# Kernel tuning notes

Measured on AMD Instinct MI355X. Metric: run time of the kernel, lower is better.

## Reference

```python
import jax, jax.numpy as jnp
import numpy as np

N = 10000
E = 640000


def setup_inputs() -> dict:
    key = jax.random.key(0)
    k = jax.random.split(key, 6)
    x = jax.random.normal(k[0], (N, 128), dtype=jnp.float32)
    edge_index = jax.random.randint(k[1], (2, E), 0, N, dtype=jnp.int64)
    # Linear weights stored as [in, out] (torch stores [out, in]; math is x @ W.T + b)
    w1 = jax.random.normal(k[2], (128, 128), dtype=jnp.float32) * 0.05
    b1 = jax.random.normal(k[3], (128,), dtype=jnp.float32) * 0.05
    w2 = jax.random.normal(k[4], (128, 128), dtype=jnp.float32) * 0.05
    b2 = jax.random.normal(k[5], (128,), dtype=jnp.float32) * 0.05
    return {"x": x, "edge_index": edge_index, "w1": w1, "b1": b1, "w2": w2, "b2": b2}


def gin_conv(x, src, dst, w, b, eps=0.0):
    # aggregate: out[i] = sum over edges (src->dst=i) of x[src]
    agg = jax.ops.segment_sum(x[src], dst, num_segments=N)  # [N, d]
    h = (1.0 + eps) * x + agg
    return h @ w + b


def reference(x, edge_index, w1, b1, w2, b2):
    src, dst = edge_index[0], edge_index[1]
    h = gin_conv(x, src, dst, w1, b1)
    h = jax.nn.relu(h)
    h = gin_conv(h, src, dst, w2, b2)
    return jax.nn.log_softmax(h, axis=1)
```

## Files before the change

kernel.cpp:

```cpp
#include <hip/hip_runtime.h>
#include <cstdint>

#define NNODES 10000
#define FDIM 128
#define MAXDEG 192
#define NPB 40
#define NBIN 256
#define BINCAP 4096
#define SENT16 0x27102710u

typedef _Float16 h2v  __attribute__((ext_vector_type(2)));
typedef _Float16 f16x8 __attribute__((ext_vector_type(8)));
typedef float    f32x4 __attribute__((ext_vector_type(4)));

__device__ __align__(16)  int            g_binoff[NBIN];
__device__ __align__(16)  unsigned       g_binbuf[NBIN * BINCAP];
__device__ __align__(16)  int            g_cnt[NNODES];
__device__ __align__(16)  unsigned short g_bkt[NNODES * MAXDEG];
__device__ __align__(256) unsigned g_xh [(NNODES + 1) * FDIM / 2];
__device__ __align__(256) unsigned g_h1h[(NNODES + 1) * FDIM / 2];
__device__ __align__(16)  unsigned g_wf[2 * 8192];

__device__ inline h2v as_h2(unsigned u) { return __builtin_bit_cast(h2v, u); }
__device__ inline unsigned as_u(h2v v) { return __builtin_bit_cast(unsigned, v); }
__device__ inline unsigned pack_f16x2(float a, float b) {
  h2v v; v[0] = (_Float16)a; v[1] = (_Float16)b;
  return as_u(v);
}
__device__ inline void vadd4(uint4& a, const uint4& b) {
  a.x = as_u(as_h2(a.x) + as_h2(b.x));
  a.y = as_u(as_h2(a.y) + as_h2(b.y));
  a.z = as_u(as_h2(a.z) + as_h2(b.z));
  a.w = as_u(as_h2(a.w) + as_h2(b.w));
}

__global__ __launch_bounds__(512) void prep1_kernel(
    const float* __restrict__ x, const int* __restrict__ ei,
    const float* __restrict__ w1, const float* __restrict__ w2,
    int E_, int PBLK) {
  const int bid = blockIdx.x, tid = threadIdx.x;
  if (bid < PBLK) {
    __shared__ int lcnt[NBIN], lbase[NBIN];
    if (tid < NBIN) lcnt[tid] = 0;
    __syncthreads();
    int dv[8], sv[8], rk[8], bn[8];
#pragma unroll
    for (int k = 0; k < 8; ++k) {
      int e = bid * 4096 + k * 512 + tid;
      dv[k] = (e < E_) ? ei[E_ + e] : -1;
      sv[k] = (e < E_) ? ei[e] : 0;
    }
#pragma unroll
    for (int k = 0; k < 8; ++k) {
      if (dv[k] >= 0) {
        bn[k] = (unsigned)dv[k] / NPB;
        rk[k] = atomicAdd(&lcnt[bn[k]], 1);
      }
    }
    __syncthreads();
    if (tid < NBIN && lcnt[tid] > 0)
      lbase[tid] = atomicAdd(&g_binoff[tid], lcnt[tid]);
    __syncthreads();
#pragma unroll
    for (int k = 0; k < 8; ++k) {
      if (dv[k] >= 0) {
        int pos = lbase[bn[k]] + rk[k];
        if (pos < BINCAP)
          g_binbuf[bn[k] * BINCAP + pos] =
              ((unsigned)(dv[k] - bn[k] * NPB) << 16) | (unsigned)sv[k];
      }
    }
  } else if (bid < PBLK + 625) {
    int i = (bid - PBLK) * 512 + tid;
    if (i < NNODES * 32) {
      float4 v = *(const float4*)(x + 4 * (size_t)i);
      uint2 o; o.x = pack_f16x2(v.x, v.y); o.y = pack_f16x2(v.z, v.w);
      *(uint2*)(g_xh + 2 * (size_t)i) = o;
    }
  } else {
    int idx = (bid - PBLK - 625) * 512 + tid;
    if (idx < 4096) {
      const float* w = (idx >= 2048) ? w2 : w1;
      int s = idx & 2047;
      int sl = s & 63, nk = s >> 6;
      int n = nk >> 2, kc = nk & 3;
      int kbase = kc * 32 + (sl >> 4) * 8;
      int f = n * 16 + (sl & 15);
      unsigned d0 = pack_f16x2(w[(size_t)(kbase + 0) * FDIM + f],
                               w[(size_t)(kbase + 1) * FDIM + f]);
      unsigned d1 = pack_f16x2(w[(size_t)(kbase + 2) * FDIM + f],
                               w[(size_t)(kbase + 3) * FDIM + f]);
      unsigned d2 = pack_f16x2(w[(size_t)(kbase + 4) * FDIM + f],
                               w[(size_t)(kbase + 5) * FDIM + f]);
      unsigned d3 = pack_f16x2(w[(size_t)(kbase + 6) * FDIM + f],
                               w[(size_t)(kbase + 7) * FDIM + f]);
      *(uint4*)(g_wf + (idx >> 11) * 8192 + 4 * s) = make_uint4(d0, d1, d2, d3);
    }
  }
}

__global__ __launch_bounds__(512) void prep2_kernel() {
  __shared__ int lcnt[NPB];
  __shared__ __align__(16) unsigned short lbkt[NPB * MAXDEG];

  const int bid = blockIdx.x, tid = threadIdx.x;
  const int lo = bid * NPB;
  const int nnr = NNODES - lo;
  const int nn = (nnr < 0) ? 0 : ((nnr < NPB) ? nnr : NPB);
  for (int i = tid; i < NPB; i += 512) lcnt[i] = 0;
  {
    const uint4 sent = make_uint4(SENT16, SENT16, SENT16, SENT16);
    uint4* lb4 = (uint4*)lbkt;
    for (int i = tid; i < NPB * MAXDEG / 8; i += 512) lb4[i] = sent;
  }
  __syncthreads();

  int cnt = g_binoff[bid];
  if (cnt > BINCAP) cnt = BINCAP;
  const unsigned* buf = g_binbuf + (size_t)bid * BINCAP;
  for (int i = tid; i < cnt; i += 512) {
    unsigned p = buf[i];
    int rel = (int)(p >> 16);
    if (rel < nn) {
      int q = atomicAdd(&lcnt[rel], 1);
      if (q < MAXDEG) lbkt[rel * MAXDEG + q] = (unsigned short)(p & 0xffffu);
    }
  }
  __syncthreads();

  for (int i = tid; i < nn; i += 512)
    g_cnt[lo + i] = (lcnt[i] > MAXDEG) ? MAXDEG : lcnt[i];
  const int nq = nn * (MAXDEG / 8);
  const uint4* srcq = (const uint4*)lbkt;
  uint4* dstq = (uint4*)(g_bkt + (size_t)lo * MAXDEG);
  for (int i = tid; i < nq; i += 512) dstq[i] = srcq[i];
  if (tid == 0) g_binoff[bid] = 0;
}

template <int MODE>
__global__ __launch_bounds__(512) void gin_layer_kernel(
    const float* __restrict__ bvec,
    float* __restrict__ out_g) {
  const unsigned* __restrict__ xh = (MODE == 0) ? g_xh : g_h1h;

  __shared__ __align__(16) unsigned al[16 * 68];
  __shared__ __align__(16) unsigned cfu[8 * 132];

  const int tid = threadIdx.x;
  const int wave = tid >> 6, lane = tid & 63;
  const int quad = lane >> 4, m16 = lane & 15;
  const int node0 = blockIdx.x * 8;
  const int myn = node0 + wave;

  const unsigned short* nb16 = g_bkt + (size_t)myn * MAXDEG;
  int idxr[3];
#pragma unroll
  for (int r = 0; r < 3; ++r)
    idxr[r] = (int)nb16[r * 64 + lane];
  const int deg = g_cnt[myn];
  uint4 self4 = *(const uint4*)(xh + (size_t)myn * 64 + (m16 << 2));

  uint4 bf[4];
  {
    const unsigned* wfp = g_wf + (MODE ? 8192 : 0);
#pragma unroll
    for (int kc = 0; kc < 4; ++kc)
      bf[kc] = *(const uint4*)(wfp + ((wave * 4 + kc) * 64 + lane) * 4);
  }
  const float bb = bvec[wave * 16 + m16];

  for (int i2 = tid; i2 < 8 * 68; i2 += 512) al[8 * 68 + i2] = 0;

  h2v a0 = as_h2(0u), a1 = as_h2(0u), a2 = as_h2(0u), a3 = as_h2(0u);
  const int nbat = (deg + 31) >> 5;
  for (int bt = 0; bt < nbat; ++bt) {
    const int r = bt >> 1;
    const int src = (r == 0) ? idxr[0] : ((r == 1) ? idxr[1] : idxr[2]);
    const int base = (bt & 1) << 5;
    uint4 t[8];
#pragma unroll
    for (int k = 0; k < 8; ++k) {
      int e = __builtin_amdgcn_ds_bpermute((base + 4 * k + quad) << 2, src);
      t[k] = *(const uint4*)(xh + (unsigned)((e << 6) | (m16 << 2)));
    }
#pragma unroll
    for (int st2 = 1; st2 < 8; st2 <<= 1)
#pragma unroll
      for (int k = 0; k < 8; k += 2 * st2) vadd4(t[k], t[k + st2]);
    a0 += as_h2(t[0].x); a1 += as_h2(t[0].y);
    a2 += as_h2(t[0].z); a3 += as_h2(t[0].w);
  }

  int rr;
  rr = __shfl_xor((int)as_u(a0), 16, 64); a0 += as_h2((unsigned)rr);
  rr = __shfl_xor((int)as_u(a0), 32, 64); a0 += as_h2((unsigned)rr);
  rr = __shfl_xor((int)as_u(a1), 16, 64); a1 += as_h2((unsigned)rr);
  rr = __shfl_xor((int)as_u(a1), 32, 64); a1 += as_h2((unsigned)rr);
  rr = __shfl_xor((int)as_u(a2), 16, 64); a2 += as_h2((unsigned)rr);
  rr = __shfl_xor((int)as_u(a2), 32, 64); a2 += as_h2((unsigned)rr);
  rr = __shfl_xor((int)as_u(a3), 16, 64); a3 += as_h2((unsigned)rr);
  rr = __shfl_xor((int)as_u(a3), 32, 64); a3 += as_h2((unsigned)rr);
  a0 += as_h2(self4.x); a1 += as_h2(self4.y);
  a2 += as_h2(self4.z); a3 += as_h2(self4.w);
  if (quad == 0)
    *(uint4*)(al + wave * 68 + (m16 << 2)) =
        make_uint4(as_u(a0), as_u(a1), as_u(a2), as_u(a3));
  __syncthreads();

  uint4 af[4];
#pragma unroll
  for (int kc = 0; kc < 4; ++kc)
    af[kc] = *(const uint4*)(al + m16 * 68 + kc * 16 + quad * 4);

  const int n = wave;
  f32x4 acc = {0.f, 0.f, 0.f, 0.f};
#pragma unroll
  for (int kc = 0; kc < 4; ++kc)
    acc = __builtin_amdgcn_mfma_f32_16x16x32_f16(
            __builtin_bit_cast(f16x8, af[kc]),
            __builtin_bit_cast(f16x8, bf[kc]), acc, 0, 0, 0);

  if (MODE == 0) {
    _Float16* ch = (_Float16*)cfu;
    const int f = n * 16 + m16;
    if (quad < 2) {
#pragma unroll
      for (int reg = 0; reg < 4; ++reg)
        ch[(quad * 4 + reg) * 136 + f] = (_Float16)fmaxf(acc[reg] + bb, 0.f);
    }
    __syncthreads();
    if (tid < 256) {
      const int row = tid >> 5, c2 = (tid & 31) * 2;
      uint2 v = *(const uint2*)(cfu + row * 68 + c2);
      *(uint2*)(&g_h1h[(size_t)(node0 + row) * 64 + c2]) = v;
    }
  } else {
    float* cf = (float*)cfu;
    const int f = n * 16 + m16;
    if (quad < 2) {
#pragma unroll
      for (int reg = 0; reg < 4; ++reg)
        cf[(quad * 4 + reg) * 132 + f] = acc[reg] + bb;
    }
    __syncthreads();
    if (tid < 256) {
      const int row = tid >> 5, li = tid & 31;
      const float* base = cf + row * 132 + li * 4;
      float4 a4 = *(const float4*)(base);
      float mx = fmaxf(fmaxf(a4.x, a4.y), fmaxf(a4.z, a4.w));
#pragma unroll
      for (int off = 16; off >= 1; off >>= 1)
        mx = fmaxf(mx, __shfl_xor(mx, off, 64));
      float s = (__expf(a4.x - mx) + __expf(a4.y - mx))
              + (__expf(a4.z - mx) + __expf(a4.w - mx));
#pragma unroll
      for (int off = 16; off >= 1; off >>= 1)
        s += __shfl_xor(s, off, 64);
      const float ls = mx + __logf(s);
      float* orow = out_g + (size_t)(node0 + row) * FDIM + li * 4;
      *(float4*)(orow) = make_float4(a4.x - ls, a4.y - ls, a4.z - ls, a4.w - ls);
    }
  }
}

extern "C" void kernel_launch(void* const* d_in, const int* in_sizes, int n_in,
                              void* d_out, int out_size, void* d_ws, size_t ws_size,
                              hipStream_t stream) {
  const float* x  = (const float*)d_in[0];
  const int*   ei = (const int*)d_in[1];
  const float* w1 = (const float*)d_in[2];
  const float* b1 = (const float*)d_in[3];
  const float* w2 = (const float*)d_in[4];
  const float* b2 = (const float*)d_in[5];
  float* out = (float*)d_out;

  const int E_ = in_sizes[1] / 2;
  const int PBLK = (E_ + 4095) / 4096;

  prep1_kernel<<<PBLK + 625 + 8, 512, 0, stream>>>(x, ei, w1, w2, E_, PBLK);
  prep2_kernel<<<NBIN, 512, 0, stream>>>();

  gin_layer_kernel<0><<<1250, 512, 0, stream>>>(b1, nullptr);
  gin_layer_kernel<1><<<1250, 512, 0, stream>>>(b2, out);
}
```

Before: 103.6 us.

## Process two nodes per wave so each block fills the full 16-row MFMA tile

Each wave now gathers and aggregates neighbours for two nodes at once, so a block covers 16 nodes instead of 8. The full 16-row MFMA A tile is used rather than half of it being zero padding, which halves the grid and the per-block weight fragment loads. Interleaving the two gathers also doubles the loads in flight per wave. In exchange, each wave runs for the larger of its two nodes' degrees, register pressure rises, and there are fewer blocks to hide latency.

After: 107.7 us. 1.04x slower.

```diff
diff --git a/kernel.cpp b/kernel.cpp
--- a/kernel.cpp
+++ b/kernel.cpp
@@ -144,21 +144,75 @@
   const unsigned* __restrict__ xh = (MODE == 0) ? g_xh : g_h1h;
 
   __shared__ __align__(16) unsigned al[16 * 68];
-  __shared__ __align__(16) unsigned cfu[8 * 132];
+  __shared__ __align__(16) unsigned cfu[16 * 132];
 
   const int tid = threadIdx.x;
   const int wave = tid >> 6, lane = tid & 63;
   const int quad = lane >> 4, m16 = lane & 15;
-  const int node0 = blockIdx.x * 8;
-  const int myn = node0 + wave;
-
-  const unsigned short* nb16 = g_bkt + (size_t)myn * MAXDEG;
-  int idxr[3];
-#pragma unroll
-  for (int r = 0; r < 3; ++r)
-    idxr[r] = (int)nb16[r * 64 + lane];
-  const int deg = g_cnt[myn];
-  uint4 self4 = *(const uint4*)(xh + (size_t)myn * 64 + (m16 << 2));
+  const int node0 = blockIdx.x * 16;
+  const int myn0 = node0 + wave * 2;
+
+  int idxr[2][3];
+#pragma unroll
+  for (int i = 0; i < 2; ++i) {
+    const unsigned short* nb16 = g_bkt + (size_t)(myn0 + i) * MAXDEG;
+#pragma unroll
+    for (int r = 0; r < 3; ++r)
+      idxr[i][r] = (int)nb16[r * 64 + lane];
+  }
+  const int2 dg2 = *(const int2*)(g_cnt + myn0);
+  uint4 self4[2];
+#pragma unroll
+  for (int i = 0; i < 2; ++i)
+    self4[i] = *(const uint4*)(xh + (size_t)(myn0 + i) * 64 + (m16 << 2));
+
+  h2v acc[2][4];
+#pragma unroll
+  for (int i = 0; i < 2; ++i)
+#pragma unroll
+    for (int j = 0; j < 4; ++j) acc[i][j] = as_h2(0u);
+
+  const int nb0 = (dg2.x + 31) >> 5, nb1 = (dg2.y + 31) >> 5;
+  const int nbmax = (nb0 > nb1) ? nb0 : nb1;
+  for (int bt = 0; bt < nbmax; ++bt) {
+    const int r = bt >> 1;
+    const int base = (bt & 1) << 5;
+    const int src0 = (r == 0) ? idxr[0][0] : ((r == 1) ? idxr[0][1] : idxr[0][2]);
+    const int src1 = (r == 0) ? idxr[1][0] : ((r == 1) ? idxr[1][1] : idxr[1][2]);
+    uint4 ta[8], tb[8];
+#pragma unroll
+    for (int k = 0; k < 8; ++k) {
+      int ea = __builtin_amdgcn_ds_bpermute((base + 4 * k + quad) << 2, src0);
+      int eb = __builtin_amdgcn_ds_bpermute((base + 4 * k + quad) << 2, src1);
+      ta[k] = *(const uint4*)(xh + (unsigned)((ea << 6) | (m16 << 2)));
+      tb[k] = *(const uint4*)(xh + (unsigned)((eb << 6) | (m16 << 2)));
+    }
+#pragma unroll
+    for (int st2 = 1; st2 < 8; st2 <<= 1)
+#pragma unroll
+      for (int k = 0; k < 8; k += 2 * st2) { vadd4(ta[k], ta[k + st2]); vadd4(tb[k], tb[k + st2]); }
+    acc[0][0] += as_h2(ta[0].x); acc[0][1] += as_h2(ta[0].y);
+    acc[0][2] += as_h2(ta[0].z); acc[0][3] += as_h2(ta[0].w);
+    acc[1][0] += as_h2(tb[0].x); acc[1][1] += as_h2(tb[0].y);
+    acc[1][2] += as_h2(tb[0].z); acc[1][3] += as_h2(tb[0].w);
+  }
+
+#pragma unroll
+  for (int i = 0; i < 2; ++i) {
+    int rr;
+#pragma unroll
+    for (int j = 0; j < 4; ++j) {
+      rr = __shfl_xor((int)as_u(acc[i][j]), 16, 64); acc[i][j] += as_h2((unsigned)rr);
+      rr = __shfl_xor((int)as_u(acc[i][j]), 32, 64); acc[i][j] += as_h2((unsigned)rr);
+    }
+    acc[i][0] += as_h2(self4[i].x); acc[i][1] += as_h2(self4[i].y);
+    acc[i][2] += as_h2(self4[i].z); acc[i][3] += as_h2(self4[i].w);
+    if (quad == 0)
+      *(uint4*)(al + (wave * 2 + i) * 68 + (m16 << 2)) =
+          make_uint4(as_u(acc[i][0]), as_u(acc[i][1]),
+                     as_u(acc[i][2]), as_u(acc[i][3]));
+  }
+  __syncthreads();
 
   uint4 bf[4];
   {
@@ -169,97 +223,51 @@
   }
   const float bb = bvec[wave * 16 + m16];
 
-  for (int i2 = tid; i2 < 8 * 68; i2 += 512) al[8 * 68 + i2] = 0;
-
-  h2v a0 = as_h2(0u), a1 = as_h2(0u), a2 = as_h2(0u), a3 = as_h2(0u);
-  const int nbat = (deg + 31) >> 5;
-  for (int bt = 0; bt < nbat; ++bt) {
-    const int r = bt >> 1;
-    const int src = (r == 0) ? idxr[0] : ((r == 1) ? idxr[1] : idxr[2]);
-    const int base = (bt & 1) << 5;
-    uint4 t[8];
-#pragma unroll
-    for (int k = 0; k < 8; ++k) {
-      int e = __builtin_amdgcn_ds_bpermute((base + 4 * k + quad) << 2, src);
-      t[k] = *(const uint4*)(xh + (unsigned)((e << 6) | (m16 << 2)));
-    }
-#pragma unroll
-    for (int st2 = 1; st2 < 8; st2 <<= 1)
-#pragma unroll
-      for (int k = 0; k < 8; k += 2 * st2) vadd4(t[k], t[k + st2]);
-    a0 += as_h2(t[0].x); a1 += as_h2(t[0].y);
-    a2 += as_h2(t[0].z); a3 += as_h2(t[0].w);
-  }
-
-  int rr;
-  rr = __shfl_xor((int)as_u(a0), 16, 64); a0 += as_h2((unsigned)rr);
-  rr = __shfl_xor((int)as_u(a0), 32, 64); a0 += as_h2((unsigned)rr);
-  rr = __shfl_xor((int)as_u(a1), 16, 64); a1 += as_h2((unsigned)rr);
-  rr = __shfl_xor((int)as_u(a1), 32, 64); a1 += as_h2((unsigned)rr);
-  rr = __shfl_xor((int)as_u(a2), 16, 64); a2 += as_h2((unsigned)rr);
-  rr = __shfl_xor((int)as_u(a2), 32, 64); a2 += as_h2((unsigned)rr);
-  rr = __shfl_xor((int)as_u(a3), 16, 64); a3 += as_h2((unsigned)rr);
-  rr = __shfl_xor((int)as_u(a3), 32, 64); a3 += as_h2((unsigned)rr);
-  a0 += as_h2(self4.x); a1 += as_h2(self4.y);
-  a2 += as_h2(self4.z); a3 += as_h2(self4.w);
-  if (quad == 0)
-    *(uint4*)(al + wave * 68 + (m16 << 2)) =
-        make_uint4(as_u(a0), as_u(a1), as_u(a2), as_u(a3));
-  __syncthreads();
-
   uint4 af[4];
 #pragma unroll
   for (int kc = 0; kc < 4; ++kc)
     af[kc] = *(const uint4*)(al + m16 * 68 + kc * 16 + quad * 4);
 
   const int n = wave;
-  f32x4 acc = {0.f, 0.f, 0.f, 0.f};
+  f32x4 acc2 = {0.f, 0.f, 0.f, 0.f};
 #pragma unroll
   for (int kc = 0; kc < 4; ++kc)
-    acc = __builtin_amdgcn_mfma_f32_16x16x32_f16(
-            __builtin_bit_cast(f16x8, af[kc]),
-            __builtin_bit_cast(f16x8, bf[kc]), acc, 0, 0, 0);
+    acc2 = __builtin_amdgcn_mfma_f32_16x16x32_f16(
+             __builtin_bit_cast(f16x8, af[kc]),
+             __builtin_bit_cast(f16x8, bf[kc]), acc2, 0, 0, 0);
 
   if (MODE == 0) {
     _Float16* ch = (_Float16*)cfu;
     const int f = n * 16 + m16;
-    if (quad < 2) {
-#pragma unroll
-      for (int reg = 0; reg < 4; ++reg)
-        ch[(quad * 4 + reg) * 136 + f] = (_Float16)fmaxf(acc[reg] + bb, 0.f);
-    }
-    __syncthreads();
-    if (tid < 256) {
-      const int row = tid >> 5, c2 = (tid & 31) * 2;
-      uint2 v = *(const uint2*)(cfu + row * 68 + c2);
-      *(uint2*)(&g_h1h[(size_t)(node0 + row) * 64 + c2]) = v;
-    }
+#pragma unroll
+    for (int reg = 0; reg < 4; ++reg)
+      ch[(quad * 4 + reg) * 136 + f] = (_Float16)fmaxf(acc2[reg] + bb, 0.f);
+    __syncthreads();
+    const int row = tid >> 5, c2 = (tid & 31) * 2;
+    uint2 v = *(const uint2*)(cfu + row * 68 + c2);
+    *(uint2*)(&g_h1h[(size_t)(node0 + row) * 64 + c2]) = v;
   } else {
     float* cf = (float*)cfu;
     const int f = n * 16 + m16;
-    if (quad < 2) {
-#pragma unroll
-      for (int reg = 0; reg < 4; ++reg)
-        cf[(quad * 4 + reg) * 132 + f] = acc[reg] + bb;
-    }
-    __syncthreads();
-    if (tid < 256) {
-      const int row = tid >> 5, li = tid & 31;
-      const float* base = cf + row * 132 + li * 4;
-      float4 a4 = *(const float4*)(base);
-      float mx = fmaxf(fmaxf(a4.x, a4.y), fmaxf(a4.z, a4.w));
-#pragma unroll
-      for (int off = 16; off >= 1; off >>= 1)
-        mx = fmaxf(mx, __shfl_xor(mx, off, 64));
-      float s = (__expf(a4.x - mx) + __expf(a4.y - mx))
-              + (__expf(a4.z - mx) + __expf(a4.w - mx));
-#pragma unroll
-      for (int off = 16; off >= 1; off >>= 1)
-        s += __shfl_xor(s, off, 64);
-      const float ls = mx + __logf(s);
-      float* orow = out_g + (size_t)(node0 + row) * FDIM + li * 4;
-      *(float4*)(orow) = make_float4(a4.x - ls, a4.y - ls, a4.z - ls, a4.w - ls);
-    }
+#pragma unroll
+    for (int reg = 0; reg < 4; ++reg)
+      cf[(quad * 4 + reg) * 132 + f] = acc2[reg] + bb;
+    __syncthreads();
+    const int row = tid >> 5, li = tid & 31;
+    const float* base = cf + row * 132 + li * 4;
+    float4 a4 = *(const float4*)(base);
+    float mx = fmaxf(fmaxf(a4.x, a4.y), fmaxf(a4.z, a4.w));
+#pragma unroll
+    for (int off = 16; off >= 1; off >>= 1)
+      mx = fmaxf(mx, __shfl_xor(mx, off, 64));
+    float s = (__expf(a4.x - mx) + __expf(a4.y - mx))
+            + (__expf(a4.z - mx) + __expf(a4.w - mx));
+#pragma unroll
+    for (int off = 16; off >= 1; off >>= 1)
+      s += __shfl_xor(s, off, 64);
+    const float ls = mx + __logf(s);
+    float* orow = out_g + (size_t)(node0 + row) * FDIM + li * 4;
+    *(float4*)(orow) = make_float4(a4.x - ls, a4.y - ls, a4.z - ls, a4.w - ls);
   }
 }
 
@@ -280,6 +288,6 @@
   prep1_kernel<<<PBLK + 625 + 8, 512, 0, stream>>>(x, ei, w1, w2, E_, PBLK);
   prep2_kernel<<<NBIN, 512, 0, stream>>>();
 
-  gin_layer_kernel<0><<<1250, 512, 0, stream>>>(b1, nullptr);
-  gin_layer_kernel<1><<<1250, 512, 0, stream>>>(b2, out);
-}
+  gin_layer_kernel<0><<<625, 512, 0, stream>>>(b1, nullptr);
+  gin_layer_kernel<1><<<625, 512, 0, stream>>>(b2, out);
+}
```
